# Performance work log

Hardware: AMD Instinct MI355X
Metric: run time of the kernel (lower is better)

Reference implementation:

```python
import jax, jax.numpy as jnp
import numpy as np

DATA_DIM = 2048
COORD_DIM = 2
NUM_V = DATA_DIM // COORD_DIM  # 1024 vertices
HID = 256
TDIM = 128
NUM_LAYERS = 4
B = 512


def _sinusoidal(t, dim=TDIM):
    half = dim // 2
    freqs = jnp.exp(-jnp.log(10000.0) * jnp.arange(half, dtype=jnp.float32) / (half - 1))
    ang = t.astype(jnp.float32)[:, None] * freqs[None, :]  # (B, half)
    return jnp.concatenate([jnp.sin(ang), jnp.cos(ang)], axis=1)  # (B, dim)


def _cycle_agg(h):
    # degree-3 cycle graph (self + next + prev), values 1/3 each == circular-shift mean
    # h: (B, V, D)
    return (h + jnp.roll(h, -1, axis=1) + jnp.roll(h, 1, axis=1)) * (1.0 / 3.0)


def setup_inputs() -> dict:
    key = jax.random.key(0)
    ks = jax.random.split(key, 16)
    dims = [COORD_DIM + TDIM] + [HID] * NUM_LAYERS  # [130,256,256,256,256]

    def glorot(k, shape):
        fan_in = shape[0]
        return jax.random.normal(k, shape, dtype=jnp.float32) / jnp.sqrt(jnp.float32(fan_in))

    inp = {
        'x': jax.random.normal(ks[0], (B, DATA_DIM), dtype=jnp.float32),
        't': jax.random.randint(ks[1], (B,), 0, 1000, dtype=jnp.int32),
        'time_W': glorot(ks[2], (TDIM, TDIM)),
        'time_b': jnp.zeros((TDIM,), jnp.float32),
        'W0': glorot(ks[3], (dims[0], dims[1])), 'b0': jnp.zeros((dims[1],), jnp.float32),
        'W1': glorot(ks[4], (dims[1], dims[2])), 'b1': jnp.zeros((dims[2],), jnp.float32),
        'W2': glorot(ks[5], (dims[2], dims[3])), 'b2': jnp.zeros((dims[3],), jnp.float32),
        'W3': glorot(ks[6], (dims[3], dims[4])), 'b3': jnp.zeros((dims[4],), jnp.float32),
        'res0_W': glorot(ks[7], (dims[0], dims[1])),
        'hW1': glorot(ks[8], (HID, HID)), 'hb1': jnp.zeros((HID,), jnp.float32),
        'hW2': glorot(ks[9], (HID, COORD_DIM)), 'hb2': jnp.zeros((COORD_DIM,), jnp.float32),
    }
    return inp


def reference(x, t, time_W, time_b, W0, b0, W1, b1, W2, b2, W3, b3, res0_W, hW1, hb1, hW2, hb2):
    silu = jax.nn.silu
    coords = x.reshape(B, NUM_V, COORD_DIM)
    temb = silu(_sinusoidal(t) @ time_W + time_b)  # (B, TDIM)
    temb = jnp.broadcast_to(temb[:, None, :], (B, NUM_V, TDIM))
    h = jnp.concatenate([coords, temb], axis=-1)  # (B, V, 130)

    Ws = [W0, W1, W2, W3]
    bs = [b0, b1, b2, b3]
    for i in range(NUM_LAYERS):
        residual = h @ res0_W if i == 0 else h
        # GraphConvolution: adj @ (h W) + b, with adj == normalized cycle aggregation
        h = _cycle_agg(h @ Ws[i]) + bs[i] + residual
        h = silu(h)

    h = silu(h @ hW1 + hb1) @ hW2 + hb2  # (B, V, 2)
    return h.reshape(B, DATA_DIM)
```

## Files before the change

### kernel.cpp

```cpp
#include <hip/hip_runtime.h>
#include <hip/hip_bf16.h>


typedef __attribute__((ext_vector_type(8))) short bf16x8;
typedef __attribute__((ext_vector_type(4))) float f32x4;

#define NV 1024

#define OFF_W0T   0
#define OFF_W1T   40960
#define OFF_W2T   106496
#define OFF_W3T   172032
#define OFF_HW1T  237568
#define OFF_HW2T  303104
#define OFF_TEMB  307200
#define PREP_ELEMS 307200

__device__ __forceinline__ float bf2f(short u){
  __hip_bfloat16 h;
  *reinterpret_cast<short*>(&h) = u;
  return __bfloat162float(h);
}
__device__ __forceinline__ short f2bf(float f){
  __hip_bfloat16 h = __float2bfloat16(f);
  return *reinterpret_cast<short*>(&h);
}
__device__ __forceinline__ float silu_f(float v){
  float e = __expf(-v);
  return v * __builtin_amdgcn_rcpf(1.f + e);
}
__device__ __forceinline__ f32x4 zero4(){ f32x4 z = {0.f,0.f,0.f,0.f}; return z; }

__global__ void prep_kernel(const float* __restrict__ W0, const float* __restrict__ res0,
                            const float* __restrict__ W1, const float* __restrict__ W2,
                            const float* __restrict__ W3, const float* __restrict__ hW1,
                            const float* __restrict__ hW2, short* __restrict__ ws){
  int idx = blockIdx.x * 256 + threadIdx.x;
  if (idx >= PREP_ELEMS) return;
  float v = 0.f;
  if (idx < 40960){
    int n = idx / 160, k = idx - n * 160;
    if (k < 128)      v = W0[(k + 2) * 256 + n] + res0[(k + 2) * 256 + n];
    else if (k < 130) v = W0[(k - 128) * 256 + n];
    else if (k < 132) v = res0[(k - 130) * 256 + n];
  } else if (idx < 303104){
    int rem = idx - 40960;
    int seg = rem >> 16;
    int r2 = rem & 65535;
    int n = r2 >> 8, k = r2 & 255;
    const float* src = (seg == 0) ? W1 : (seg == 1) ? W2 : (seg == 2) ? W3 : hW1;
    v = src[k * 256 + n];
    if (seg < 3) v *= (1.f / 3.f);
  } else {
    int rem = idx - 303104;
    int n = rem >> 8, k = rem & 255;
    if (n < 2) v = hW2[k * 2 + n];
  }
  ws[idx] = f2bf(v);
}

__global__ void temb_kernel(const int* __restrict__ t, const float* __restrict__ tW,
                            const float* __restrict__ tb, short* __restrict__ temb){
  __shared__ float sc[128];
  int b = blockIdx.x, n = threadIdx.x;
  float tv = (float)t[b];
  {
    int j = n & 63;
    float fr = __expf(-9.210340371976184f * (float)j * (1.f / 63.f));
    float ang = tv * fr;
    sc[n] = (n < 64) ? sinf(ang) : cosf(ang);
  }
  __syncthreads();
  float acc = tb[n];
  #pragma unroll 8
  for (int k = 0; k < 128; ++k) acc += sc[k] * tW[k * 128 + n];
  temb[b * 128 + n] = f2bf(silu_f(acc));
}

template<int KPAD>
__device__ __forceinline__ void mm2(const char* hb, const short* __restrict__ Wt,
                                    int m15, int g, int n0, f32x4 acc[5][2]){
  const short* wb = Wt + (n0 + m15) * KPAD + g * 8;
  #pragma unroll 2
  for (int ks = 0; ks < KPAD / 32; ++ks){
    bf16x8 bf0 = *(const bf16x8*)(wb + ks * 32);
    bf16x8 bf1 = *(const bf16x8*)(wb + 16 * KPAD + ks * 32);
    const int kb = ks * 64 + g * 16;
    #pragma unroll
    for (int mt = 0; mt < 5; ++mt){
      const int row = mt * 16 + m15;
      bf16x8 a = *(const bf16x8*)(hb + row * 512 + (kb ^ ((row & 7) << 4)));
      acc[mt][0] = __builtin_amdgcn_mfma_f32_16x16x32_bf16(a, bf0, acc[mt][0], 0, 0, 0);
      acc[mt][1] = __builtin_amdgcn_mfma_f32_16x16x32_bf16(a, bf1, acc[mt][1], 0, 0, 0);
    }
  }
}

__global__ __launch_bounds__(512, 4)
void gcn_fused(const float* __restrict__ x, const short* __restrict__ ws,
               const float* __restrict__ b0p, const float* __restrict__ b1p,
               const float* __restrict__ b2p, const float* __restrict__ b3p,
               const float* __restrict__ hb1p, const float* __restrict__ hb2p,
               float* __restrict__ out){
  extern __shared__ char hb[];
  const int tid = threadIdx.x;
  const int lane = tid & 63, wid = tid >> 6;
  const int m15 = lane & 15, g = lane >> 4;
  const int n0 = wid * 32;
  const int b = blockIdx.y, v0 = blockIdx.x * 64;

  {
    const short* tembp = ws + OFF_TEMB + b * 128;
    for (int task = tid; task < 72 * 16; task += 512){
      int r = task >> 4, ck = (task & 15) * 16;
      *(bf16x8*)(hb + r * 512 + (ck ^ ((r & 7) << 4))) =
          *(const bf16x8*)(tembp + (task & 15) * 8);
    }
    for (int task = tid; task < 80 * 8; task += 512){
      int r = task >> 3, q = task & 7;
      bf16x8 v = {0, 0, 0, 0, 0, 0, 0, 0};
      if (q == 0 && r < 72){
        const float* xb = x + b * 2048;
        int vm = (v0 + r - 5) & (NV - 1);
        int vc = (v0 + r - 4) & (NV - 1);
        int vp = (v0 + r - 3) & (NV - 1);
        float c0m = xb[vm * 2], c1m = xb[vm * 2 + 1];
        float c0c = xb[vc * 2], c1c = xb[vc * 2 + 1];
        float c0p = xb[vp * 2], c1p = xb[vp * 2 + 1];
        v[0] = f2bf((c0m + c0c + c0p) * (1.f / 3.f));
        v[1] = f2bf((c1m + c1c + c1p) * (1.f / 3.f));
        v[2] = f2bf(c0c);
        v[3] = f2bf(c1c);
      }
      *(bf16x8*)(hb + r * 512 + (((16 + q) * 16) ^ ((r & 7) << 4))) = v;
    }
  }
  __syncthreads();

  f32x4 acc[5][2];

  {
    #pragma unroll
    for (int mt = 0; mt < 5; ++mt){ acc[mt][0] = zero4(); acc[mt][1] = zero4(); }
    mm2<160>(hb, ws + OFF_W0T, m15, g, n0, acc);
    __syncthreads();
    const float bias[2] = { b0p[n0 + m15], b0p[n0 + 16 + m15] };
    #pragma unroll
    for (int mt = 0; mt < 5; ++mt)
      #pragma unroll
      for (int nt = 0; nt < 2; ++nt){
        const int row = mt * 16 + g * 4;
        const int cb = (n0 + nt * 16 + m15) * 2;
        #pragma unroll
        for (int j = 0; j < 4; ++j){
          short q = f2bf(silu_f(acc[mt][nt][j] + bias[nt]));
          *(short*)(hb + (row + j) * 512 + (cb ^ (((row + j) & 7) << 4))) = q;
        }
      }
  }
  __syncthreads();

  #pragma unroll
  for (int L = 0; L < 3; ++L){
    const short* Wt = ws + (L == 0 ? OFF_W1T : L == 1 ? OFF_W2T : OFF_W3T);
    const float* bp = (L == 0 ? b1p : L == 1 ? b2p : b3p);
    #pragma unroll
    for (int mt = 0; mt < 5; ++mt){ acc[mt][0] = zero4(); acc[mt][1] = zero4(); }
    mm2<256>(hb, Wt, m15, g, n0, acc);
    __syncthreads();
    const float bias[2] = { bp[n0 + m15], bp[n0 + 16 + m15] };
    #pragma unroll
    for (int mt = 0; mt < 5; ++mt)
      #pragma unroll
      for (int nt = 0; nt < 2; ++nt){
        float a0 = acc[mt][nt][0], a1 = acc[mt][nt][1];
        float a2 = acc[mt][nt][2], a3 = acc[mt][nt][3];
        float upv = (g == 3) ? acc[mt > 0 ? mt - 1 : 0][nt][3] : a3;
        float pm0 = __shfl(upv, (lane + 48) & 63);
        float dnv = (g == 0) ? acc[mt < 4 ? mt + 1 : 4][nt][0] : a0;
        float pp3 = __shfl(dnv, (lane + 16) & 63);
        float base = bias[nt];
        const int row = mt * 16 + g * 4;
        const int cb = (n0 + nt * 16 + m15) * 2;
        float r0 = bf2f(*(const short*)(hb + (row    ) * 512 + (cb ^ (((row    ) & 7) << 4))));
        float r1 = bf2f(*(const short*)(hb + (row + 1) * 512 + (cb ^ (((row + 1) & 7) << 4))));
        float r2 = bf2f(*(const short*)(hb + (row + 2) * 512 + (cb ^ (((row + 2) & 7) << 4))));
        float r3 = bf2f(*(const short*)(hb + (row + 3) * 512 + (cb ^ (((row + 3) & 7) << 4))));
        float s0 = pm0 + a0 + a1 + base + r0;
        float s1 = a0 + a1 + a2 + base + r1;
        float s2 = a1 + a2 + a3 + base + r2;
        float s3 = a2 + a3 + pp3 + base + r3;
        *(short*)(hb + (row    ) * 512 + (cb ^ (((row    ) & 7) << 4))) = f2bf(silu_f(s0));
        *(short*)(hb + (row + 1) * 512 + (cb ^ (((row + 1) & 7) << 4))) = f2bf(silu_f(s1));
        *(short*)(hb + (row + 2) * 512 + (cb ^ (((row + 2) & 7) << 4))) = f2bf(silu_f(s2));
        *(short*)(hb + (row + 3) * 512 + (cb ^ (((row + 3) & 7) << 4))) = f2bf(silu_f(s3));
      }
    __syncthreads();
  }

  {
    #pragma unroll
    for (int mt = 0; mt < 5; ++mt){ acc[mt][0] = zero4(); acc[mt][1] = zero4(); }
    mm2<256>(hb, ws + OFF_HW1T, m15, g, n0, acc);
    __syncthreads();
    const float bias[2] = { hb1p[n0 + m15], hb1p[n0 + 16 + m15] };
    #pragma unroll
    for (int mt = 0; mt < 5; ++mt)
      #pragma unroll
      for (int nt = 0; nt < 2; ++nt){
        const int row = mt * 16 + g * 4;
        const int cb = (n0 + nt * 16 + m15) * 2;
        #pragma unroll
        for (int j = 0; j < 4; ++j){
          short q = f2bf(silu_f(acc[mt][nt][j] + bias[nt]));
          *(short*)(hb + (row + j) * 512 + (cb ^ (((row + j) & 7) << 4))) = q;
        }
      }
    __syncthreads();
  }

  if (wid == 0){
    f32x4 a2[5];
    #pragma unroll
    for (int mt = 0; mt < 5; ++mt) a2[mt] = zero4();
    const short* wb = ws + OFF_HW2T + m15 * 256 + g * 8;
    #pragma unroll 2
    for (int ks = 0; ks < 8; ++ks){
      bf16x8 bfr = *(const bf16x8*)(wb + ks * 32);
      const int kb = ks * 64 + g * 16;
      #pragma unroll
      for (int mt = 0; mt < 5; ++mt){
        const int row = mt * 16 + m15;
        bf16x8 a = *(const bf16x8*)(hb + row * 512 + (kb ^ ((row & 7) << 4)));
        a2[mt] = __builtin_amdgcn_mfma_f32_16x16x32_bf16(a, bfr, a2[mt], 0, 0, 0);
      }
    }
    if (m15 < 2){
      float bias = hb2p[m15];
      #pragma unroll
      for (int mt = 0; mt < 5; ++mt)
        #pragma unroll
        for (int j = 0; j < 4; ++j){
          int row = mt * 16 + g * 4 + j;
          if (row >= 4 && row < 68)
            out[b * 2048 + (v0 + row - 4) * 2 + m15] = a2[mt][j] + bias;
        }
    }
  }
}

extern "C" void kernel_launch(void* const* d_in, const int* in_sizes, int n_in,
                              void* d_out, int out_size, void* d_ws, size_t ws_size,
                              hipStream_t stream){
  const float* x   = (const float*)d_in[0];
  const int*   t   = (const int*)  d_in[1];
  const float* tW  = (const float*)d_in[2];
  const float* tb  = (const float*)d_in[3];
  const float* W0  = (const float*)d_in[4];
  const float* b0  = (const float*)d_in[5];
  const float* W1  = (const float*)d_in[6];
  const float* b1  = (const float*)d_in[7];
  const float* W2  = (const float*)d_in[8];
  const float* b2  = (const float*)d_in[9];
  const float* W3  = (const float*)d_in[10];
  const float* b3  = (const float*)d_in[11];
  const float* res0= (const float*)d_in[12];
  const float* hW1 = (const float*)d_in[13];
  const float* hb1 = (const float*)d_in[14];
  const float* hW2 = (const float*)d_in[15];
  const float* hb2 = (const float*)d_in[16];
  short* ws  = (short*)d_ws;
  float* out = (float*)d_out;

  hipFuncSetAttribute((const void*)gcn_fused,
                      hipFuncAttributeMaxDynamicSharedMemorySize, 40960);

  prep_kernel<<<dim3((PREP_ELEMS + 255) / 256), dim3(256), 0, stream>>>(
      W0, res0, W1, W2, W3, hW1, hW2, ws);
  temb_kernel<<<dim3(512), dim3(128), 0, stream>>>(t, tW, tb, ws + OFF_TEMB);
  gcn_fused<<<dim3(16, 512), dim3(512), 40960, stream>>>(
      x, ws, b0, b1, b2, b3, hb1, hb2, out);
}
```

Measured before the change: 791.2 us.

## Ping-pong LDS activation buffers and keep residuals in registers

Activations now alternate between two LDS buffers. This removes the barrier that previously separated each layer's MFMA reads from its epilogue writes. Residual values for the skip connection stay packed in registers instead of being re-read from LDS, and bf16-to-float conversion becomes a plain shift. The cost is double the dynamic LDS per block (80 KB) plus extra registers, which likely halves blocks per CU and lowers occupancy.

```diff
diff --git a/kernel.cpp b/kernel.cpp
--- a/kernel.cpp
+++ b/kernel.cpp
@@ -17,9 +17,9 @@
 #define PREP_ELEMS 307200
 
 __device__ __forceinline__ float bf2f(short u){
-  __hip_bfloat16 h;
-  *reinterpret_cast<short*>(&h) = u;
-  return __bfloat162float(h);
+  union { unsigned int i; float f; } v;
+  v.i = ((unsigned int)(unsigned short)u) << 16;
+  return v.f;
 }
 __device__ __forceinline__ short f2bf(float f){
   __hip_bfloat16 h = __float2bfloat16(f);
@@ -78,7 +78,7 @@
 }
 
 template<int KPAD>
-__device__ __forceinline__ void mm2(const char* hb, const short* __restrict__ Wt,
+__device__ __forceinline__ void mm2(const char* hbuf, const short* __restrict__ Wt,
                                     int m15, int g, int n0, f32x4 acc[5][2]){
   const short* wb = Wt + (n0 + m15) * KPAD + g * 8;
   #pragma unroll 2
@@ -89,7 +89,7 @@
     #pragma unroll
     for (int mt = 0; mt < 5; ++mt){
       const int row = mt * 16 + m15;
-      bf16x8 a = *(const bf16x8*)(hb + row * 512 + (kb ^ ((row & 7) << 4)));
+      bf16x8 a = *(const bf16x8*)(hbuf + row * 512 + (kb ^ ((row & 7) << 4)));
       acc[mt][0] = __builtin_amdgcn_mfma_f32_16x16x32_bf16(a, bf0, acc[mt][0], 0, 0, 0);
       acc[mt][1] = __builtin_amdgcn_mfma_f32_16x16x32_bf16(a, bf1, acc[mt][1], 0, 0, 0);
     }
@@ -102,7 +102,9 @@
                const float* __restrict__ b2p, const float* __restrict__ b3p,
                const float* __restrict__ hb1p, const float* __restrict__ hb2p,
                float* __restrict__ out){
-  extern __shared__ char hb[];
+  extern __shared__ char lds[];
+  char* const hA = lds;
+  char* const hB = lds + 40960;
   const int tid = threadIdx.x;
   const int lane = tid & 63, wid = tid >> 6;
   const int m15 = lane & 15, g = lane >> 4;
@@ -113,7 +115,7 @@
     const short* tembp = ws + OFF_TEMB + b * 128;
     for (int task = tid; task < 72 * 16; task += 512){
       int r = task >> 4, ck = (task & 15) * 16;
-      *(bf16x8*)(hb + r * 512 + (ck ^ ((r & 7) << 4))) =
+      *(bf16x8*)(hA + r * 512 + (ck ^ ((r & 7) << 4))) =
           *(const bf16x8*)(tembp + (task & 15) * 8);
     }
     for (int task = tid; task < 80 * 8; task += 512){
@@ -132,43 +134,50 @@
         v[2] = f2bf(c0c);
         v[3] = f2bf(c1c);
       }
-      *(bf16x8*)(hb + r * 512 + (((16 + q) * 16) ^ ((r & 7) << 4))) = v;
+      *(bf16x8*)(hA + r * 512 + (((16 + q) * 16) ^ ((r & 7) << 4))) = v;
     }
   }
   __syncthreads();
 
   f32x4 acc[5][2];
-
-  {
+  unsigned int hreg[5][2][2];
+
+  {
+    const float bias0 = b0p[n0 + m15], bias1 = b0p[n0 + 16 + m15];
     #pragma unroll
     for (int mt = 0; mt < 5; ++mt){ acc[mt][0] = zero4(); acc[mt][1] = zero4(); }
-    mm2<160>(hb, ws + OFF_W0T, m15, g, n0, acc);
-    __syncthreads();
-    const float bias[2] = { b0p[n0 + m15], b0p[n0 + 16 + m15] };
+    mm2<160>(hA, ws + OFF_W0T, m15, g, n0, acc);
     #pragma unroll
     for (int mt = 0; mt < 5; ++mt)
       #pragma unroll
       for (int nt = 0; nt < 2; ++nt){
+        const float base = nt ? bias1 : bias0;
         const int row = mt * 16 + g * 4;
         const int cb = (n0 + nt * 16 + m15) * 2;
-        #pragma unroll
-        for (int j = 0; j < 4; ++j){
-          short q = f2bf(silu_f(acc[mt][nt][j] + bias[nt]));
-          *(short*)(hb + (row + j) * 512 + (cb ^ (((row + j) & 7) << 4))) = q;
-        }
+        unsigned short q0 = (unsigned short)f2bf(silu_f(acc[mt][nt][0] + base));
+        unsigned short q1 = (unsigned short)f2bf(silu_f(acc[mt][nt][1] + base));
+        unsigned short q2 = (unsigned short)f2bf(silu_f(acc[mt][nt][2] + base));
+        unsigned short q3 = (unsigned short)f2bf(silu_f(acc[mt][nt][3] + base));
+        *(short*)(hB + (row    ) * 512 + (cb ^ (((row    ) & 7) << 4))) = (short)q0;
+        *(short*)(hB + (row + 1) * 512 + (cb ^ (((row + 1) & 7) << 4))) = (short)q1;
+        *(short*)(hB + (row + 2) * 512 + (cb ^ (((row + 2) & 7) << 4))) = (short)q2;
+        *(short*)(hB + (row + 3) * 512 + (cb ^ (((row + 3) & 7) << 4))) = (short)q3;
+        hreg[mt][nt][0] = (unsigned int)q0 | ((unsigned int)q1 << 16);
+        hreg[mt][nt][1] = (unsigned int)q2 | ((unsigned int)q3 << 16);
       }
   }
   __syncthreads();
 
   #pragma unroll
   for (int L = 0; L < 3; ++L){
+    const char* bin  = (L & 1) ? hA : hB;
+    char*       bout = (L & 1) ? hB : hA;
     const short* Wt = ws + (L == 0 ? OFF_W1T : L == 1 ? OFF_W2T : OFF_W3T);
     const float* bp = (L == 0 ? b1p : L == 1 ? b2p : b3p);
+    const float bias0 = bp[n0 + m15], bias1 = bp[n0 + 16 + m15];
     #pragma unroll
     for (int mt = 0; mt < 5; ++mt){ acc[mt][0] = zero4(); acc[mt][1] = zero4(); }
-    mm2<256>(hb, Wt, m15, g, n0, acc);
-    __syncthreads();
-    const float bias[2] = { bp[n0 + m15], bp[n0 + 16 + m15] };
+    mm2<256>(bin, Wt, m15, g, n0, acc);
     #pragma unroll
     for (int mt = 0; mt < 5; ++mt)
       #pragma unroll
@@ -179,41 +188,47 @@
         float pm0 = __shfl(upv, (lane + 48) & 63);
         float dnv = (g == 0) ? acc[mt < 4 ? mt + 1 : 4][nt][0] : a0;
         float pp3 = __shfl(dnv, (lane + 16) & 63);
-        float base = bias[nt];
-        const int row = mt * 16 + g * 4;
-        const int cb = (n0 + nt * 16 + m15) * 2;
-        float r0 = bf2f(*(const short*)(hb + (row    ) * 512 + (cb ^ (((row    ) & 7) << 4))));
-        float r1 = bf2f(*(const short*)(hb + (row + 1) * 512 + (cb ^ (((row + 1) & 7) << 4))));
-        float r2 = bf2f(*(const short*)(hb + (row + 2) * 512 + (cb ^ (((row + 2) & 7) << 4))));
-        float r3 = bf2f(*(const short*)(hb + (row + 3) * 512 + (cb ^ (((row + 3) & 7) << 4))));
+        const float base = nt ? bias1 : bias0;
+        float r0 = bf2f((short)(hreg[mt][nt][0] & 0xffff));
+        float r1 = bf2f((short)(hreg[mt][nt][0] >> 16));
+        float r2 = bf2f((short)(hreg[mt][nt][1] & 0xffff));
+        float r3 = bf2f((short)(hreg[mt][nt][1] >> 16));
         float s0 = pm0 + a0 + a1 + base + r0;
         float s1 = a0 + a1 + a2 + base + r1;
         float s2 = a1 + a2 + a3 + base + r2;
         float s3 = a2 + a3 + pp3 + base + r3;
-        *(short*)(hb + (row    ) * 512 + (cb ^ (((row    ) & 7) << 4))) = f2bf(silu_f(s0));
-        *(short*)(hb + (row + 1) * 512 + (cb ^ (((row + 1) & 7) << 4))) = f2bf(silu_f(s1));
-        *(short*)(hb + (row + 2) * 512 + (cb ^ (((row + 2) & 7) << 4))) = f2bf(silu_f(s2));
-        *(short*)(hb + (row + 3) * 512 + (cb ^ (((row + 3) & 7) << 4))) = f2bf(silu_f(s3));
+        unsigned short q0 = (unsigned short)f2bf(silu_f(s0));
+        unsigned short q1 = (unsigned short)f2bf(silu_f(s1));
+        unsigned short q2 = (unsigned short)f2bf(silu_f(s2));
+        unsigned short q3 = (unsigned short)f2bf(silu_f(s3));
+        const int row = mt * 16 + g * 4;
+        const int cb = (n0 + nt * 16 + m15) * 2;
+        *(short*)(bout + (row    ) * 512 + (cb ^ (((row    ) & 7) << 4))) = (short)q0;
+        *(short*)(bout + (row + 1) * 512 + (cb ^ (((row + 1) & 7) << 4))) = (short)q1;
+        *(short*)(bout + (row + 2) * 512 + (cb ^ (((row + 2) & 7) << 4))) = (short)q2;
+        *(short*)(bout + (row + 3) * 512 + (cb ^ (((row + 3) & 7) << 4))) = (short)q3;
+        hreg[mt][nt][0] = (unsigned int)q0 | ((unsigned int)q1 << 16);
+        hreg[mt][nt][1] = (unsigned int)q2 | ((unsigned int)q3 << 16);
       }
     __syncthreads();
   }
 
   {
+    const float bias0 = hb1p[n0 + m15], bias1 = hb1p[n0 + 16 + m15];
     #pragma unroll
     for (int mt = 0; mt < 5; ++mt){ acc[mt][0] = zero4(); acc[mt][1] = zero4(); }
-    mm2<256>(hb, ws + OFF_HW1T, m15, g, n0, acc);
-    __syncthreads();
-    const float bias[2] = { hb1p[n0 + m15], hb1p[n0 + 16 + m15] };
+    mm2<256>(hA, ws + OFF_HW1T, m15, g, n0, acc);
     #pragma unroll
     for (int mt = 0; mt < 5; ++mt)
       #pragma unroll
       for (int nt = 0; nt < 2; ++nt){
+        const float base = nt ? bias1 : bias0;
         const int row = mt * 16 + g * 4;
         const int cb = (n0 + nt * 16 + m15) * 2;
         #pragma unroll
         for (int j = 0; j < 4; ++j){
-          short q = f2bf(silu_f(acc[mt][nt][j] + bias[nt]));
-          *(short*)(hb + (row + j) * 512 + (cb ^ (((row + j) & 7) << 4))) = q;
+          short q = f2bf(silu_f(acc[mt][nt][j] + base));
+          *(short*)(hB + (row + j) * 512 + (cb ^ (((row + j) & 7) << 4))) = q;
         }
       }
     __syncthreads();
@@ -231,7 +246,7 @@
       #pragma unroll
       for (int mt = 0; mt < 5; ++mt){
         const int row = mt * 16 + m15;
-        bf16x8 a = *(const bf16x8*)(hb + row * 512 + (kb ^ ((row & 7) << 4)));
+        bf16x8 a = *(const bf16x8*)(hB + row * 512 + (kb ^ ((row & 7) << 4)));
         a2[mt] = __builtin_amdgcn_mfma_f32_16x16x32_bf16(a, bfr, a2[mt], 0, 0, 0);
       }
     }
@@ -273,11 +288,11 @@
   float* out = (float*)d_out;
 
   hipFuncSetAttribute((const void*)gcn_fused,
-                      hipFuncAttributeMaxDynamicSharedMemorySize, 40960);
+                      hipFuncAttributeMaxDynamicSharedMemorySize, 81920);
 
   prep_kernel<<<dim3((PREP_ELEMS + 255) / 256), dim3(256), 0, stream>>>(
       W0, res0, W1, W2, W3, hW1, hW2, ws);
   temb_kernel<<<dim3(512), dim3(128), 0, stream>>>(t, tW, tb, ws + OFF_TEMB);
-  gcn_fused<<<dim3(16, 512), dim3(512), 40960, stream>>>(
+  gcn_fused<<<dim3(16, 512), dim3(512), 81920, stream>>>(
       x, ws, b0, b1, b2, b3, hb1, hb2, out);
 }
```

Result: slower. 1.085 ms (+37.1%).
